# Optimization experiments

Measured on AMD Instinct MI355X. Metric: run time of the kernel, lower is better.

## Reference

```python
import jax, jax.numpy as jnp
import numpy as np

N_NODES, N_EDGES, N_GRAPHS = 500000, 2000000, 16384


def _lin(key, fan_in, fan_out):
    # torch nn.Linear default init: U(-1/sqrt(fan_in), 1/sqrt(fan_in))
    s = 1.0 / np.sqrt(fan_in)
    kw, kb = jax.random.split(key)
    W = jax.random.uniform(kw, (fan_in, fan_out), jnp.float32, -s, s)
    b = jax.random.uniform(kb, (fan_out,), jnp.float32, -s, s)
    return W, b


def setup_inputs() -> dict:
    key = jax.random.key(0)
    ks = jax.random.split(key, 16)
    x = jax.random.normal(ks[0], (N_NODES, 131), jnp.float32)
    edge_src = jax.random.randint(ks[1], (N_EDGES,), 0, N_NODES, jnp.int32)
    edge_dst = jax.random.randint(ks[2], (N_EDGES,), 0, N_NODES, jnp.int32)
    batch_index = jnp.sort(jax.random.randint(ks[3], (N_NODES,), 0, N_GRAPHS, jnp.int32))
    solvent_descriptors = jax.random.normal(ks[4], (N_GRAPHS, 11), jnp.float32)
    Wc1, bc1 = _lin(ks[5], 131, 128)
    Wc2, bc2 = _lin(ks[6], 128, 64)
    W1, b1 = _lin(ks[7], 64 + 11, 2048)
    W2, b2 = _lin(ks[8], 2048, 1024)
    W3, b3 = _lin(ks[9], 1024, 128)
    # 6 property heads, stacked: Linear(128,32) -> ReLU -> Linear(32,1)
    Wh1 = jnp.stack([_lin(jax.random.fold_in(ks[10], i), 128, 32)[0] for i in range(6)])
    bh1 = jnp.stack([_lin(jax.random.fold_in(ks[10], i), 128, 32)[1] for i in range(6)])
    Wh2 = jnp.stack([_lin(jax.random.fold_in(ks[11], i), 32, 1)[0] for i in range(6)])
    bh2 = jnp.stack([_lin(jax.random.fold_in(ks[11], i), 32, 1)[1] for i in range(6)])
    return dict(x=x, edge_src=edge_src, edge_dst=edge_dst, batch_index=batch_index,
                solvent_descriptors=solvent_descriptors,
                Wc1=Wc1, bc1=bc1, Wc2=Wc2, bc2=bc2,
                W1=W1, b1=b1, W2=W2, b2=b2, W3=W3, b3=b3,
                Wh1=Wh1, bh1=bh1, Wh2=Wh2, bh2=bh2,
                num_graphs=N_GRAPHS)


def _gcn_conv(x, W, b, src, dst, n_nodes):
    # PyG GCNConv: add self-loops, symmetric normalization, scatter-add aggregate.
    h = x @ W                                           # [N, F_out]
    deg = jnp.zeros((n_nodes,), x.dtype).at[dst].add(1.0) + 1.0  # +1 for self-loop
    dinv = jax.lax.rsqrt(deg)                            # deg >= 1
    norm = dinv[src] * dinv[dst]                         # [E]
    agg = jnp.zeros_like(h).at[dst].add(norm[:, None] * h[src])
    agg = agg + h * (dinv * dinv)[:, None]               # self-loop contribution
    return agg + b


def reference(x, edge_src, edge_dst, batch_index, solvent_descriptors,
              Wc1, bc1, Wc2, bc2, W1, b1, W2, b2, W3, b3,
              Wh1, bh1, Wh2, bh2, num_graphs):
    n = x.shape[0]
    h = jax.nn.relu(_gcn_conv(x, Wc1, bc1, edge_src, edge_dst, n))
    h = _gcn_conv(h, Wc2, bc2, edge_src, edge_dst, n)
    g = jax.ops.segment_sum(h, batch_index, num_segments=num_graphs)  # global sum pool [G,64]
    z = jnp.concatenate([g, solvent_descriptors], axis=1)             # [G,75]
    z = jax.nn.relu(z @ W1 + b1)   # dropout is identity in eval
    z = jax.nn.relu(z @ W2 + b2)
    z = jax.nn.relu(z @ W3 + b3)   # [G,128]
    a = jax.nn.relu(jnp.einsum('gf,hfk->ghk', z, Wh1) + bh1)          # [G,6,32]
    out = jnp.einsum('ghk,hk->gh', a, Wh2[..., 0]) + bh2[:, 0]        # [G,6]
    return out
```

## Files before the change

kernel.cpp:

```cpp
#include <hip/hip_runtime.h>

#define N_NODES 500000
#define N_EDGES 2000000
#define N_GRAPHS 16384
#define STRIP 16
#define KC1 192

#define SCAN_ELEMS 2048
#define SCAN_NBLK ((N_NODES + SCAN_ELEMS - 1) / SCAN_ELEMS)

typedef short bf16x8 __attribute__((ext_vector_type(8)));
typedef float f32x4 __attribute__((ext_vector_type(4)));
typedef unsigned short u16x8 __attribute__((ext_vector_type(8)));

__device__ __forceinline__ unsigned short f2bf_rne(float x) {
    unsigned int b = __float_as_uint(x);
    unsigned int r = (b + 0x7fffu + ((b >> 16) & 1u)) >> 16;
    return (unsigned short)r;
}
__device__ __forceinline__ float bf2f(unsigned short h) {
    return __uint_as_float(((unsigned int)h) << 16);
}
__device__ __forceinline__ void split_bf(float v, unsigned short& hi, unsigned short& lo) {
    hi = f2bf_rne(v);
    lo = f2bf_rne(v - bf2f(hi));
}

__global__ __launch_bounds__(256) void k_zero2(int* counts, float* P) {
    int i = blockIdx.x * 256 + threadIdx.x;
    if (i < N_NODES) counts[i] = 0;
    if (i < N_GRAPHS * 128) P[i] = 0.0f;
}

__global__ __launch_bounds__(256) void k_hist(const int* __restrict__ dst, int* __restrict__ counts) {
    int e = blockIdx.x * 256 + threadIdx.x;
    if (e < N_EDGES) atomicAdd(&counts[dst[e]], 1);
}
__global__ __launch_bounds__(256) void k_scan_reduce(const int* __restrict__ counts, int* __restrict__ bsum) {
    int b = blockIdx.x, t = threadIdx.x;
    int base_i = b * SCAN_ELEMS + t * 8;
    int s = 0;
    #pragma unroll
    for (int j = 0; j < 8; j++) { int i = base_i + j; if (i < N_NODES) s += counts[i]; }
    __shared__ int sh[256];
    sh[t] = s; __syncthreads();
    for (int off = 128; off > 0; off >>= 1) { if (t < off) sh[t] += sh[t + off]; __syncthreads(); }
    if (t == 0) bsum[b] = sh[0];
}
__global__ __launch_bounds__(256) void k_scan_bsum(const int* __restrict__ bsum, int* __restrict__ boff,
                                                   int* __restrict__ row_ptr) {
    __shared__ int sh[256];
    int t = threadIdx.x;
    int v = (t < SCAN_NBLK) ? bsum[t] : 0;
    sh[t] = v; __syncthreads();
    for (int off = 1; off < 256; off <<= 1) {
        int u = (t >= off) ? sh[t - off] : 0;
        __syncthreads();
        sh[t] += u; __syncthreads();
    }
    boff[t] = sh[t] - v;
    if (t == 255) row_ptr[N_NODES] = sh[255];
}
__global__ __launch_bounds__(256) void k_scan_final(const int* __restrict__ counts, const int* __restrict__ boff,
                                                    int* __restrict__ row_ptr, int* __restrict__ cursor,
                                                    float* __restrict__ dinv) {
    __shared__ int sh[256];
    int b = blockIdx.x, t = threadIdx.x;
    int base_i = b * SCAN_ELEMS + t * 8;
    int c[8]; int tsum = 0;
    #pragma unroll
    for (int j = 0; j < 8; j++) {
        int i = base_i + j;
        c[j] = (i < N_NODES) ? counts[i] : 0;
        tsum += c[j];
    }
    sh[t] = tsum; __syncthreads();
    for (int off = 1; off < 256; off <<= 1) {
        int u = (t >= off) ? sh[t - off] : 0;
        __syncthreads();
        sh[t] += u; __syncthreads();
    }
    int run = boff[b] + sh[t] - tsum;
    #pragma unroll
    for (int j = 0; j < 8; j++) {
        int i = base_i + j;
        if (i < N_NODES) {
            row_ptr[i] = run;
            cursor[i]  = run;
            dinv[i]    = rsqrtf((float)c[j] + 1.0f);
        }
        run += c[j];
    }
}
__global__ __launch_bounds__(256) void k_fill(const int* __restrict__ esrc, const int* __restrict__ edst,
                                              int* __restrict__ cursor, int* __restrict__ srcs) {
    int e = blockIdx.x * 256 + threadIdx.x;
    if (e >= N_EDGES) return;
    int d = edst[e];
    int pos = atomicAdd(&cursor[d], 1);
    srcs[pos] = esrc[e];
}
__global__ __launch_bounds__(256) void k_gstart(const int* __restrict__ batch, int* __restrict__ gstart) {
    int g = blockIdx.x * 256 + threadIdx.x;
    if (g > N_GRAPHS) return;
    if (g == N_GRAPHS) { gstart[g] = N_NODES; return; }
    int lo = 0, hi = N_NODES;
    while (lo < hi) { int mid = (lo + hi) >> 1; if (batch[mid] < g) lo = mid + 1; else hi = mid; }
    gstart[g] = lo;
}

__global__ __launch_bounds__(256) void k_wprep(const float* __restrict__ Wc1, const float* __restrict__ W1,
                                               const float* __restrict__ Wh1, const float* __restrict__ bh1,
                                               unsigned short* __restrict__ c1h, unsigned short* __restrict__ c1l,
                                               unsigned short* __restrict__ w1h, unsigned short* __restrict__ w1l,
                                               unsigned short* __restrict__ whh, unsigned short* __restrict__ whl,
                                               float* __restrict__ bh1p) {
    int idx = blockIdx.x * 256 + threadIdx.x;
    if (idx < 24576) {
        int c = idx / KC1, k = idx % KC1;
        float v = (k < 131) ? Wc1[(size_t)k * 128 + c] : 0.0f;
        unsigned short hi, lo; split_bf(v, hi, lo);
        c1h[idx] = hi; c1l[idx] = lo;
    } else if (idx < 24576 + 262144) {
        int i = idx - 24576;
        int n = i >> 7, k = i & 127;
        float v = (k < 75) ? W1[(size_t)k * 2048 + n] : 0.0f;
        unsigned short hi, lo; split_bf(v, hi, lo);
        w1h[i] = hi; w1l[i] = lo;
    } else if (idx < 24576 + 262144 + 32768) {
        int i = idx - 24576 - 262144;
        int c = i >> 7, f = i & 127;
        float v = 0.0f;
        if (c < 192) v = Wh1[(c >> 5) * (128 * 32) + f * 32 + (c & 31)];
        unsigned short hi, lo; split_bf(v, hi, lo);
        whh[i] = hi; whl[i] = lo;
    } else if (idx < 24576 + 262144 + 32768 + 256) {
        int i = idx - 24576 - 262144 - 32768;
        bh1p[i] = (i < 192) ? bh1[i] : 0.0f;
    }
}

__device__ __forceinline__ void conv1_loadA(const float* __restrict__ X, int bm, int w, int l,
                                            int koffg, int kt, u16x8* a_st) {
    const int k0 = kt * 64;
    #pragma unroll
    for (int i = 0; i < 8; i++) {
        int row = bm * 128 + w * 64 + i * 8 + (l >> 3);
        if (row >= N_NODES) row = N_NODES - 1;
        const float* src = X + (size_t)row * 131 + k0 + koffg;
        #pragma unroll
        for (int j = 0; j < 8; j++) {
            int k = k0 + koffg + j;
            a_st[i][j] = (k < 131) ? f2bf_rne(src[j]) : (unsigned short)0;
        }
    }
}

__global__ __launch_bounds__(256) void k_mfma_conv1(const float* __restrict__ X,
                                                    const unsigned short* __restrict__ Bh,
                                                    const unsigned short* __restrict__ Bl,
                                                    const float* __restrict__ dinv,
                                                    unsigned short* __restrict__ C) {
    __shared__ short lds[24576];
    const int tid = threadIdx.x;
    const int w = tid >> 6, l = tid & 63;
    const int bm = blockIdx.x;
    const int wm = w >> 1, wn = w & 1;
    const int lane15 = l & 15, lg = l >> 4, l7 = l & 7;
    const int koffg = ((l & 7) ^ ((l >> 3) & 7)) * 8;
    f32x4 acc[4][4] = {};
    u16x8 a_st[8];
    if (w < 2) conv1_loadA(X, bm, w, l, koffg, 0, a_st);
    #pragma unroll
    for (int kt = 0; kt < 3; kt++) {
        const int k0 = kt * 64;
        __syncthreads();
        if (w < 2) {
            #pragma unroll
            for (int i = 0; i < 8; i++)
                *(u16x8*)&lds[w * 4096 + i * 512 + l * 8] = a_st[i];
            if (kt < 2) conv1_loadA(X, bm, w, l, koffg, kt + 1, a_st);
        } else {
            const unsigned short* gB = (w == 2) ? Bh : Bl;
            #pragma unroll
            for (int i = 0; i < 16; i++) {
                int row = i * 8 + (l >> 3);
                const unsigned short* src = gB + (size_t)row * KC1 + k0 + koffg;
                __builtin_amdgcn_global_load_lds(
                    (const __attribute__((address_space(1))) unsigned int*)src,
                    (__attribute__((address_space(3))) unsigned int*)&lds[(w - 1) * 8192 + i * 512],
                    16, 0, 0);
            }
        }
        __syncthreads();
        #pragma unroll
        for (int kh = 0; kh < 2; kh++) {
            const int slot = ((kh * 4 + lg) ^ l7) * 8;
            bf16x8 af[4], bhf[4], blf[4];
            #pragma unroll
            for (int m = 0; m < 4; m++)
                af[m] = *(const bf16x8*)&lds[(wm * 64 + m * 16 + lane15) * 64 + slot];
            #pragma unroll
            for (int n = 0; n < 4; n++) {
                int si = (wn * 64 + n * 16 + lane15) * 64 + slot;
                bhf[n] = *(const bf16x8*)&lds[8192 + si];
                blf[n] = *(const bf16x8*)&lds[16384 + si];
            }
            #pragma unroll
            for (int m = 0; m < 4; m++)
                #pragma unroll
                for (int n = 0; n < 4; n++) {
                    acc[m][n] = __builtin_amdgcn_mfma_f32_16x16x32_bf16(af[m], bhf[n], acc[m][n], 0, 0, 0);
                    acc[m][n] = __builtin_amdgcn_mfma_f32_16x16x32_bf16(af[m], blf[n], acc[m][n], 0, 0, 0);
                }
        }
    }
    const size_t row_b = (size_t)bm * 128 + wm * 64 + lg * 4;
    const int col_b = wn * 64 + lane15;
    #pragma unroll
    for (int m = 0; m < 4; m++) {
        #pragma unroll
        for (int j = 0; j < 4; j++) {
            size_t row = row_b + m * 16 + j;
            if (row < N_NODES) {
                float dn = dinv[row];
                #pragma unroll
                for (int n = 0; n < 4; n++)
                    C[row * 128 + col_b + n * 16] = f2bf_rne(dn * acc[m][n][j]);
            }
        }
    }
}

__global__ __launch_bounds__(256) void k_gather1(const unsigned short* __restrict__ h,
                                                 const float* __restrict__ dinv,
                                                 const float* __restrict__ bias,
                                                 const int* __restrict__ row_ptr, const int* __restrict__ srcs,
                                                 unsigned short* __restrict__ r1) {
    int g = blockIdx.x * 256 + threadIdx.x;
    int n = g >> 6, lane = g & 63;
    if (n >= N_NODES) return;
    int c = lane * 2;
    unsigned int hv = *(const unsigned int*)(h + (size_t)n * 128 + c);
    float t0 = bf2f((unsigned short)(hv & 0xffffu));
    float t1 = bf2f((unsigned short)(hv >> 16));
    int e0 = row_ptr[n], e1 = row_ptr[n + 1];
    int e = e0;
    for (; e + 4 <= e1; e += 4) {
        int sA = srcs[e], sB = srcs[e + 1], sC = srcs[e + 2], sD = srcs[e + 3];
        unsigned int hA = *(const unsigned int*)(h + (size_t)sA * 128 + c);
        unsigned int hB = *(const unsigned int*)(h + (size_t)sB * 128 + c);
        unsigned int hC = *(const unsigned int*)(h + (size_t)sC * 128 + c);
        unsigned int hD = *(const unsigned int*)(h + (size_t)sD * 128 + c);
        t0 += bf2f((unsigned short)(hA & 0xffffu));
        t1 += bf2f((unsigned short)(hA >> 16));
        t0 += bf2f((unsigned short)(hB & 0xffffu));
        t1 += bf2f((unsigned short)(hB >> 16));
        t0 += bf2f((unsigned short)(hC & 0xffffu));
        t1 += bf2f((unsigned short)(hC >> 16));
        t0 += bf2f((unsigned short)(hD & 0xffffu));
        t1 += bf2f((unsigned short)(hD >> 16));
    }
    for (; e < e1; e++) {
        int sA = srcs[e];
        unsigned int hA = *(const unsigned int*)(h + (size_t)sA * 128 + c);
        t0 += bf2f((unsigned short)(hA & 0xffffu));
        t1 += bf2f((unsigned short)(hA >> 16));
    }
    float dn = dinv[n];
    float a0 = fmaxf(fmaf(dn, t0, bias[c]), 0.0f);
    float a1 = fmaxf(fmaf(dn, t1, bias[c + 1]), 0.0f);
    unsigned int o = (unsigned int)f2bf_rne(dn * a0) | ((unsigned int)f2bf_rne(dn * a1) << 16);
    *(unsigned int*)(r1 + (size_t)n * 128 + c) = o;
}

__global__ __launch_bounds__(256) void k_g2p(const unsigned short* __restrict__ r1,
                                             const float* __restrict__ dinv,
                                             const int* __restrict__ row_ptr, const int* __restrict__ srcs,
                                             const int* __restrict__ batch,
                                             float* __restrict__ P) {
    int gw = (blockIdx.x * 256 + threadIdx.x) >> 6;
    int lane = threadIdx.x & 63;
    if (gw >= N_NODES / STRIP) return;
    int n0 = gw * STRIP;
    int c = lane * 2;
    float a0 = 0.0f, a1 = 0.0f;
    int cur_g = batch[n0];
    for (int n = n0; n < n0 + STRIP; n++) {
        int bg = batch[n];
        if (bg != cur_g) {
            atomicAdd(&P[(size_t)cur_g * 128 + c], a0);
            atomicAdd(&P[(size_t)cur_g * 128 + c + 1], a1);
            a0 = a1 = 0.0f;
            cur_g = bg;
        }
        unsigned int hv = *(const unsigned int*)(r1 + (size_t)n * 128 + c);
        float u0 = bf2f((unsigned short)(hv & 0xffffu));
        float u1 = bf2f((unsigned short)(hv >> 16));
        int e0 = row_ptr[n], e1 = row_ptr[n + 1];
        int e = e0;
        for (; e + 4 <= e1; e += 4) {
            int sA = srcs[e], sB = srcs[e + 1], sC = srcs[e + 2], sD = srcs[e + 3];
            unsigned int hA = *(const unsigned int*)(r1 + (size_t)sA * 128 + c);
            unsigned int hB = *(const unsigned int*)(r1 + (size_t)sB * 128 + c);
            unsigned int hC = *(const unsigned int*)(r1 + (size_t)sC * 128 + c);
            unsigned int hD = *(const unsigned int*)(r1 + (size_t)sD * 128 + c);
            u0 += bf2f((unsigned short)(hA & 0xffffu));
            u1 += bf2f((unsigned short)(hA >> 16));
            u0 += bf2f((unsigned short)(hB & 0xffffu));
            u1 += bf2f((unsigned short)(hB >> 16));
            u0 += bf2f((unsigned short)(hC & 0xffffu));
            u1 += bf2f((unsigned short)(hC >> 16));
            u0 += bf2f((unsigned short)(hD & 0xffffu));
            u1 += bf2f((unsigned short)(hD >> 16));
        }
        for (; e < e1; e++) {
            int sA = srcs[e];
            unsigned int hA = *(const unsigned int*)(r1 + (size_t)sA * 128 + c);
            u0 += bf2f((unsigned short)(hA & 0xffffu));
            u1 += bf2f((unsigned short)(hA >> 16));
        }
        float dn = dinv[n];
        a0 = fmaf(dn, u0, a0);
        a1 = fmaf(dn, u1, a1);
    }
    atomicAdd(&P[(size_t)cur_g * 128 + c], a0);
    atomicAdd(&P[(size_t)cur_g * 128 + c + 1], a1);
}

__global__ __launch_bounds__(128) void k_zg(const float* __restrict__ P, const int* __restrict__ gstart,
                                            const float* __restrict__ Wc2, const float* __restrict__ bc2,
                                            const float* __restrict__ solv,
                                            unsigned short* __restrict__ z0h, unsigned short* __restrict__ z0l) {
    int g = blockIdx.x; int c = threadIdx.x;
    float v = 0.0f;
    if (c < 64) {
        const float* pr = P + (size_t)g * 128;
        float s = 0.0f;
        #pragma unroll 8
        for (int k = 0; k < 128; k++) s = fmaf(pr[k], Wc2[k * 64 + c], s);
        v = s + (float)(gstart[g + 1] - gstart[g]) * bc2[c];
    } else if (c < 75) {
        v = solv[g * 11 + (c - 64)];
    }
    unsigned short hi, lo; split_bf(v, hi, lo);
    z0h[(size_t)g * 128 + c] = hi;
    z0l[(size_t)g * 128 + c] = lo;
}

__global__ __launch_bounds__(256) void k_tsplit(const float* __restrict__ W, int R, int C,
                                                unsigned short* __restrict__ Th, unsigned short* __restrict__ Tl) {
    __shared__ float tile[64][65];
    int cb = blockIdx.x * 64, rb = blockIdx.y * 64;
    int tc = threadIdx.x & 63, tr4 = threadIdx.x >> 6;
    #pragma unroll 4
    for (int i = 0; i < 16; i++) {
        int r = tr4 + i * 4;
        tile[r][tc] = W[(size_t)(rb + r) * C + cb + tc];
    }
    __syncthreads();
    #pragma unroll 4
    for (int i = 0; i < 16; i++) {
        int r = tr4 + i * 4;
        float v = tile[tc][r];
        unsigned short hi, lo; split_bf(v, hi, lo);
        size_t o = (size_t)(cb + r) * R + rb + tc;
        Th[o] = hi; Tl[o] = lo;
    }
}

template<int OMODE>
__global__ __launch_bounds__(256) void k_mfma_split(
        const unsigned short* __restrict__ Ah, const unsigned short* __restrict__ Al,
        const unsigned short* __restrict__ Bh, const unsigned short* __restrict__ Bl,
        const float* __restrict__ bias,
        float* __restrict__ C, unsigned short* __restrict__ Ch, unsigned short* __restrict__ Cl,
        int N, int K) {
    __shared__ short lds[32768];
    const int tid = threadIdx.x;
    const int w = tid >> 6, l = tid & 63;
    const int nwg = gridDim.x;
    const int q = nwg >> 3;
    const int id0 = blockIdx.x;
    const int id = (id0 & 7) * q + (id0 >> 3);
    const int bm = id & 127;
    const int bn = id >> 7;
    const unsigned short* gmat = (w == 0) ? Ah : (w == 1) ? Al : (w == 2) ? Bh : Bl;
    const size_t grow0 = (size_t)((w < 2) ? bm : bn) * 128 + (l >> 3);
    const int koffg = ((l & 7) ^ ((l >> 3) & 7)) * 8;
    const int ldsw = w * 8192;
    const int wm = w >> 1, wn = w & 1;
    const int lane15 = l & 15, lg = l >> 4, l7 = l & 7;
    f32x4 acc[4][4] = {};
    const int NK = K >> 6;
    for (int kt = 0; kt < NK; kt++) {
        const int k0 = kt << 6;
        __syncthreads();
        #pragma unroll
        for (int i = 0; i < 16; i++) {
            const unsigned short* src = gmat + (grow0 + (size_t)i * 8) * (size_t)K + k0 + koffg;
            __builtin_amdgcn_global_load_lds(
                (const __attribute__((address_space(1))) unsigned int*)src,
                (__attribute__((address_space(3))) unsigned int*)&lds[ldsw + i * 512],
                16, 0, 0);
        }
        __syncthreads();
        #pragma unroll
        for (int kh = 0; kh < 2; kh++) {
            const int slot = ((kh * 4 + lg) ^ l7) * 8;
            bf16x8 ahf[4], alf[4], bhf[4], blf[4];
            #pragma unroll
            for (int m = 0; m < 4; m++) {
                int si = (wm * 64 + m * 16 + lane15) * 64 + slot;
                ahf[m] = *(const bf16x8*)&lds[si];
                alf[m] = *(const bf16x8*)&lds[8192 + si];
            }
            #pragma unroll
            for (int n = 0; n < 4; n++) {
                int si = (wn * 64 + n * 16 + lane15) * 64 + slot;
                bhf[n] = *(const bf16x8*)&lds[16384 + si];
                blf[n] = *(const bf16x8*)&lds[24576 + si];
            }
            #pragma unroll
            for (int m = 0; m < 4; m++)
                #pragma unroll
                for (int n = 0; n < 4; n++) {
                    acc[m][n] = __builtin_amdgcn_mfma_f32_16x16x32_bf16(ahf[m], bhf[n], acc[m][n], 0, 0, 0);
                    acc[m][n] = __builtin_amdgcn_mfma_f32_16x16x32_bf16(ahf[m], blf[n], acc[m][n], 0, 0, 0);
                    acc[m][n] = __builtin_amdgcn_mfma_f32_16x16x32_bf16(alf[m], bhf[n], acc[m][n], 0, 0, 0);
                }
        }
    }
    const int row_b = bm * 128 + wm * 64 + lg * 4;
    const int col_b = bn * 128 + wn * 64 + lane15;
    #pragma unroll
    for (int m = 0; m < 4; m++)
        #pragma unroll
        for (int n = 0; n < 4; n++) {
            int col = col_b + n * 16;
            float bv = bias[col];
            #pragma unroll
            for (int j = 0; j < 4; j++) {
                int row = row_b + m * 16 + j;
                float v = fmaxf(acc[m][n][j] + bv, 0.0f);
                size_t o = (size_t)row * N + col;
                if (OMODE == 0) {
                    C[o] = v;
                } else {
                    unsigned short hi, lo; split_bf(v, hi, lo);
                    Ch[o] = hi; Cl[o] = lo;
                }
            }
        }
}

__global__ __launch_bounds__(256) void k_heads_out(const float* __restrict__ a,
                                                   const float* __restrict__ Wh2,
                                                   const float* __restrict__ bh2,
                                                   float* __restrict__ out) {
    int i = blockIdx.x * 256 + threadIdx.x;
    if (i >= N_GRAPHS * 6) return;
    int g = i / 6, h = i % 6;
    const float* ap = a + (size_t)g * 256 + h * 32;
    const float* wp = Wh2 + h * 32;
    float s = 0.0f;
    #pragma unroll
    for (int k = 0; k < 32; k++) s = fmaf(ap[k], wp[k], s);
    out[i] = s + bh2[h];
}

extern "C" void kernel_launch(void* const* d_in, const int* in_sizes, int n_in,
                              void* d_out, int out_size, void* d_ws, size_t ws_size,
                              hipStream_t stream) {
    const float* x    = (const float*)d_in[0];
    const int*   esrc = (const int*)d_in[1];
    const int*   edst = (const int*)d_in[2];
    const int*   batch= (const int*)d_in[3];
    const float* solv = (const float*)d_in[4];
    const float* Wc1  = (const float*)d_in[5];
    const float* bc1  = (const float*)d_in[6];
    const float* Wc2  = (const float*)d_in[7];
    const float* bc2  = (const float*)d_in[8];
    const float* W1   = (const float*)d_in[9];
    const float* b1   = (const float*)d_in[10];
    const float* W2   = (const float*)d_in[11];
    const float* b2   = (const float*)d_in[12];
    const float* W3   = (const float*)d_in[13];
    const float* b3   = (const float*)d_in[14];
    const float* Wh1  = (const float*)d_in[15];
    const float* bh1  = (const float*)d_in[16];
    const float* Wh2  = (const float*)d_in[17];
    const float* bh2  = (const float*)d_in[18];
    float* out = (float*)d_out;

    float* ws    = (float*)d_ws;
    float* bufA  = ws;
    float* bufB  = bufA + 64000000;
    float* dinv  = bufB + 64000000;
    float* bh1p  = dinv + 524288;
    int* counts  = (int*)(bh1p + 256);
    int* row_ptr = counts + N_NODES;
    int* cursor  = row_ptr + 500224;
    int* srcs    = cursor + N_NODES;
    int* bsum    = srcs + N_EDGES;
    int* boff    = bsum + 256;
    int* gstart  = boff + 256;
    float* P     = bufB + 61902848;

    unsigned short* h_bf = (unsigned short*)bufA;
    unsigned short* r1   = (unsigned short*)bufB;
    unsigned short* wc1h = (unsigned short*)(bufA + 60000000);
    unsigned short* wc1l = wc1h + 128 * KC1;

    unsigned short* z1h  = (unsigned short*)bufB;
    unsigned short* z1l  = (unsigned short*)(bufB + 16800000);
    unsigned short* z2h  = (unsigned short*)bufA;
    unsigned short* z2l  = (unsigned short*)(bufA + 8400000);
    unsigned short* z3h  = (unsigned short*)(bufB + 34000000);
    unsigned short* z3l  = (unsigned short*)(bufB + 35100000);
    unsigned short* w2th = (unsigned short*)(bufA + 33000000);
    unsigned short* w2tl = (unsigned short*)(bufA + 34100000);
    unsigned short* w3th = (unsigned short*)(bufA + 35200000);
    unsigned short* w3tl = (unsigned short*)(bufA + 35300000);
    float* ab = bufA + 36000000;
    unsigned short* z0h  = (unsigned short*)(bufA + 41000000);
    unsigned short* z0l  = (unsigned short*)(bufA + 42100000);
    unsigned short* w1th = (unsigned short*)(bufA + 43200000);
    unsigned short* w1tl = (unsigned short*)(bufA + 43400000);
    unsigned short* whh  = (unsigned short*)(bufA + 43600000);
    unsigned short* whl  = (unsigned short*)(bufA + 43700000);

    k_zero2<<<(N_GRAPHS * 128 + 255) / 256, 256, 0, stream>>>(counts, P);
    k_hist<<<(N_EDGES + 255) / 256, 256, 0, stream>>>(edst, counts);
    k_scan_reduce<<<SCAN_NBLK, 256, 0, stream>>>(counts, bsum);
    k_scan_bsum<<<1, 256, 0, stream>>>(bsum, boff, row_ptr);
    k_scan_final<<<SCAN_NBLK, 256, 0, stream>>>(counts, boff, row_ptr, cursor, dinv);
    k_fill<<<(N_EDGES + 255) / 256, 256, 0, stream>>>(esrc, edst, cursor, srcs);
    k_gstart<<<(N_GRAPHS + 256) / 256, 256, 0, stream>>>(batch, gstart);

    k_wprep<<<(319744 + 255) / 256, 256, 0, stream>>>(Wc1, W1, Wh1, bh1,
                                                      wc1h, wc1l, w1th, w1tl, whh, whl, bh1p);

    k_mfma_conv1<<<(N_NODES + 127) / 128, 256, 0, stream>>>(x, wc1h, wc1l, dinv, h_bf);

    k_gather1<<<(N_NODES * 64) / 256, 256, 0, stream>>>(h_bf, dinv, bc1, row_ptr, srcs, r1);

    k_g2p<<<((N_NODES / STRIP) * 64 + 255) / 256, 256, 0, stream>>>(r1, dinv, row_ptr, srcs, batch, P);

    k_tsplit<<<dim3(1024 / 64, 2048 / 64), 256, 0, stream>>>(W2, 2048, 1024, w2th, w2tl);
    k_tsplit<<<dim3(128 / 64, 1024 / 64), 256, 0, stream>>>(W3, 1024, 128, w3th, w3tl);

    k_zg<<<N_GRAPHS, 128, 0, stream>>>(P, gstart, Wc2, bc2, solv, z0h, z0l);

    k_mfma_split<1><<<(2048 / 128) * (N_GRAPHS / 128), 256, 0, stream>>>(
        z0h, z0l, w1th, w1tl, b1, nullptr, z1h, z1l, 2048, 128);
    k_mfma_split<1><<<(1024 / 128) * (N_GRAPHS / 128), 256, 0, stream>>>(
        z1h, z1l, w2th, w2tl, b2, nullptr, z2h, z2l, 1024, 2048);
    k_mfma_split<1><<<(128 / 128) * (N_GRAPHS / 128), 256, 0, stream>>>(
        z2h, z2l, w3th, w3tl, b3, nullptr, z3h, z3l, 128, 1024);
    k_mfma_split<0><<<(256 / 128) * (N_GRAPHS / 128), 256, 0, stream>>>(
        z3h, z3l, whh, whl, bh1p, ab, nullptr, nullptr, 256, 128);

    k_heads_out<<<(N_GRAPHS * 6 + 255) / 256, 256, 0, stream>>>(ab, Wh2, bh2, out);
}
```

Baseline: 1.103 ms.

## Split GCN gather and pooling into two feature-half passes

Each of the two sparse aggregation kernels (conv1 gather and the conv2 gather fused with pooling) now takes a template parameter selecting one 64-column half of the 128 features. They are launched twice, half 0 then half 1, with one bf16 element per lane instead of two. The aim is to halve the footprint of the randomly gathered feature rows in each pass so the neighbour rows stay cached better. The cost is reading the CSR indices and row pointers twice, narrower 2-byte loads, and twice as many launches.

```diff
diff --git a/kernel.cpp b/kernel.cpp
--- a/kernel.cpp
+++ b/kernel.cpp
@@ -232,6 +232,7 @@
     }
 }
 
+template<int HALF>
 __global__ __launch_bounds__(256) void k_gather1(const unsigned short* __restrict__ h,
                                                  const float* __restrict__ dinv,
                                                  const float* __restrict__ bias,
@@ -240,40 +241,28 @@
     int g = blockIdx.x * 256 + threadIdx.x;
     int n = g >> 6, lane = g & 63;
     if (n >= N_NODES) return;
-    int c = lane * 2;
-    unsigned int hv = *(const unsigned int*)(h + (size_t)n * 128 + c);
-    float t0 = bf2f((unsigned short)(hv & 0xffffu));
-    float t1 = bf2f((unsigned short)(hv >> 16));
+    int c = HALF * 64 + lane;
+    float t = bf2f(h[(size_t)n * 128 + c]);
     int e0 = row_ptr[n], e1 = row_ptr[n + 1];
     int e = e0;
     for (; e + 4 <= e1; e += 4) {
         int sA = srcs[e], sB = srcs[e + 1], sC = srcs[e + 2], sD = srcs[e + 3];
-        unsigned int hA = *(const unsigned int*)(h + (size_t)sA * 128 + c);
-        unsigned int hB = *(const unsigned int*)(h + (size_t)sB * 128 + c);
-        unsigned int hC = *(const unsigned int*)(h + (size_t)sC * 128 + c);
-        unsigned int hD = *(const unsigned int*)(h + (size_t)sD * 128 + c);
-        t0 += bf2f((unsigned short)(hA & 0xffffu));
-        t1 += bf2f((unsigned short)(hA >> 16));
-        t0 += bf2f((unsigned short)(hB & 0xffffu));
-        t1 += bf2f((unsigned short)(hB >> 16));
-        t0 += bf2f((unsigned short)(hC & 0xffffu));
-        t1 += bf2f((unsigned short)(hC >> 16));
-        t0 += bf2f((unsigned short)(hD & 0xffffu));
-        t1 += bf2f((unsigned short)(hD >> 16));
+        float hA = bf2f(h[(size_t)sA * 128 + c]);
+        float hB = bf2f(h[(size_t)sB * 128 + c]);
+        float hC = bf2f(h[(size_t)sC * 128 + c]);
+        float hD = bf2f(h[(size_t)sD * 128 + c]);
+        t += hA; t += hB; t += hC; t += hD;
     }
     for (; e < e1; e++) {
         int sA = srcs[e];
-        unsigned int hA = *(const unsigned int*)(h + (size_t)sA * 128 + c);
-        t0 += bf2f((unsigned short)(hA & 0xffffu));
-        t1 += bf2f((unsigned short)(hA >> 16));
+        t += bf2f(h[(size_t)sA * 128 + c]);
     }
     float dn = dinv[n];
-    float a0 = fmaxf(fmaf(dn, t0, bias[c]), 0.0f);
-    float a1 = fmaxf(fmaf(dn, t1, bias[c + 1]), 0.0f);
-    unsigned int o = (unsigned int)f2bf_rne(dn * a0) | ((unsigned int)f2bf_rne(dn * a1) << 16);
-    *(unsigned int*)(r1 + (size_t)n * 128 + c) = o;
-}
-
+    float a = fmaxf(fmaf(dn, t, bias[c]), 0.0f);
+    r1[(size_t)n * 128 + c] = f2bf_rne(dn * a);
+}
+
+template<int HALF>
 __global__ __launch_bounds__(256) void k_g2p(const unsigned short* __restrict__ r1,
                                              const float* __restrict__ dinv,
                                              const int* __restrict__ row_ptr, const int* __restrict__ srcs,
@@ -283,49 +272,34 @@
     int lane = threadIdx.x & 63;
     if (gw >= N_NODES / STRIP) return;
     int n0 = gw * STRIP;
-    int c = lane * 2;
-    float a0 = 0.0f, a1 = 0.0f;
+    int c = HALF * 64 + lane;
+    float a = 0.0f;
     int cur_g = batch[n0];
     for (int n = n0; n < n0 + STRIP; n++) {
         int bg = batch[n];
         if (bg != cur_g) {
-            atomicAdd(&P[(size_t)cur_g * 128 + c], a0);
-            atomicAdd(&P[(size_t)cur_g * 128 + c + 1], a1);
-            a0 = a1 = 0.0f;
+            atomicAdd(&P[(size_t)cur_g * 128 + c], a);
+            a = 0.0f;
             cur_g = bg;
         }
-        unsigned int hv = *(const unsigned int*)(r1 + (size_t)n * 128 + c);
-        float u0 = bf2f((unsigned short)(hv & 0xffffu));
-        float u1 = bf2f((unsigned short)(hv >> 16));
+        float u = bf2f(r1[(size_t)n * 128 + c]);
         int e0 = row_ptr[n], e1 = row_ptr[n + 1];
         int e = e0;
         for (; e + 4 <= e1; e += 4) {
             int sA = srcs[e], sB = srcs[e + 1], sC = srcs[e + 2], sD = srcs[e + 3];
-            unsigned int hA = *(const unsigned int*)(r1 + (size_t)sA * 128 + c);
-            unsigned int hB = *(const unsigned int*)(r1 + (size_t)sB * 128 + c);
-            unsigned int hC = *(const unsigned int*)(r1 + (size_t)sC * 128 + c);
-            unsigned int hD = *(const unsigned int*)(r1 + (size_t)sD * 128 + c);
-            u0 += bf2f((unsigned short)(hA & 0xffffu));
-            u1 += bf2f((unsigned short)(hA >> 16));
-            u0 += bf2f((unsigned short)(hB & 0xffffu));
-            u1 += bf2f((unsigned short)(hB >> 16));
-            u0 += bf2f((unsigned short)(hC & 0xffffu));
-            u1 += bf2f((unsigned short)(hC >> 16));
-            u0 += bf2f((unsigned short)(hD & 0xffffu));
-            u1 += bf2f((unsigned short)(hD >> 16));
+            float hA = bf2f(r1[(size_t)sA * 128 + c]);
+            float hB = bf2f(r1[(size_t)sB * 128 + c]);
+            float hC = bf2f(r1[(size_t)sC * 128 + c]);
+            float hD = bf2f(r1[(size_t)sD * 128 + c]);
+            u += hA; u += hB; u += hC; u += hD;
         }
         for (; e < e1; e++) {
             int sA = srcs[e];
-            unsigned int hA = *(const unsigned int*)(r1 + (size_t)sA * 128 + c);
-            u0 += bf2f((unsigned short)(hA & 0xffffu));
-            u1 += bf2f((unsigned short)(hA >> 16));
-        }
-        float dn = dinv[n];
-        a0 = fmaf(dn, u0, a0);
-        a1 = fmaf(dn, u1, a1);
-    }
-    atomicAdd(&P[(size_t)cur_g * 128 + c], a0);
-    atomicAdd(&P[(size_t)cur_g * 128 + c + 1], a1);
+            u += bf2f(r1[(size_t)sA * 128 + c]);
+        }
+        a = fmaf(dinv[n], u, a);
+    }
+    atomicAdd(&P[(size_t)cur_g * 128 + c], a);
 }
 
 __global__ __launch_bounds__(128) void k_zg(const float* __restrict__ P, const int* __restrict__ gstart,
@@ -543,9 +517,12 @@
 
     k_mfma_conv1<<<(N_NODES + 127) / 128, 256, 0, stream>>>(x, wc1h, wc1l, dinv, h_bf);
 
-    k_gather1<<<(N_NODES * 64) / 256, 256, 0, stream>>>(h_bf, dinv, bc1, row_ptr, srcs, r1);
-
-    k_g2p<<<((N_NODES / STRIP) * 64 + 255) / 256, 256, 0, stream>>>(r1, dinv, row_ptr, srcs, batch, P);
+    const int gather_grid = (N_NODES * 64) / 256;
+    const int g2p_grid = ((N_NODES / STRIP) * 64 + 255) / 256;
+    k_gather1<0><<<gather_grid, 256, 0, stream>>>(h_bf, dinv, bc1, row_ptr, srcs, r1);
+    k_g2p<0><<<g2p_grid, 256, 0, stream>>>(r1, dinv, row_ptr, srcs, batch, P);
+    k_gather1<1><<<gather_grid, 256, 0, stream>>>(h_bf, dinv, bc1, row_ptr, srcs, r1);
+    k_g2p<1><<<g2p_grid, 256, 0, stream>>>(r1, dinv, row_ptr, srcs, batch, P);
 
     k_tsplit<<<dim3(1024 / 64, 2048 / 64), 256, 0, stream>>>(W2, 2048, 1024, w2th, w2tl);
     k_tsplit<<<dim3(128 / 64, 1024 / 64), 256, 0, stream>>>(W3, 1024, 128, w3th, w3tl);
```

Result: slower. 1.410 ms (+27.8%).
